# Optimization experiments

Hardware: AMD Instinct MI355X
Metric: run time of the kernel (lower is better)

Reference implementation:

```python
import jax, jax.numpy as jnp
import numpy as np
from jax.scipy.special import erf

N = 512          # n_points
S = 64           # steps
M = 32768        # number of events
MAX_TIME = 100.0
DELTA = MAX_TIME / S   # time_delta_size (torch.linspace gives uniform deltas)
EPS = 1e-12


def setup_inputs() -> dict:
    key = jax.random.key(0)
    k1, k2, k3, k4 = jax.random.split(key, 4)
    times = jnp.sort(jax.random.uniform(k1, (M,), dtype=jnp.float32) * MAX_TIME)
    ij = jax.random.randint(k2, (M, 2), 0, N).astype(jnp.float32)
    data = jnp.concatenate([ij, times[:, None]], axis=1)  # [node_i, node_j, time]
    z0 = jax.random.uniform(k3, (N, 2), dtype=jnp.float32) * 0.5
    v0 = jax.random.uniform(k4, (N, 2, S), dtype=jnp.float32) * 0.5
    beta = jnp.ones((1, 1), dtype=jnp.float32)
    return {
        "data": data,
        "t0": jnp.zeros((1,), dtype=jnp.float32),
        "tn": jnp.full((1,), MAX_TIME, dtype=jnp.float32),
        "z0": z0,
        "v0": v0,
        "beta": beta,
    }


def _forward(data, z0, v0, beta):
    times = data[:, 2]                      # (M,) assumed sorted, in [0, MAX_TIME]
    b = beta[0, 0]

    # --- time-step bucketing (vectorized version of the Python list-comp/np.unique) ---
    step_f = jnp.floor(times / DELTA)       # floored step value
    idx = jnp.clip(step_f, 0, S - 1).astype(jnp.int32)  # 't if t < steps else t-1'

    # piecewise-constant-velocity cumulative positions: (N, 2, S+1)
    Z_steps = jnp.concatenate(
        [z0[:, :, None], z0[:, :, None] + jnp.cumsum(v0 * DELTA, axis=2)], axis=2
    )

    # latent positions at each event time: (N, 2, M)
    dd = times - step_f * DELTA             # offset within the step
    Zt = Z_steps[:, :, idx] + v0[:, :, idx] * dd

    # --- event intensity: sum_{i<j} sum_e (beta - ||Zt_i - Zt_j||^2) ---
    # sum over events of d_ij computed via one small-K GEMM instead of (N,N,M)
    G = jnp.einsum('ndm,kdm->nk', Zt, Zt)   # (N, N)
    sq = jnp.diagonal(G)                    # sum_{d,m} Zt_i^2
    Dsum = sq[:, None] + sq[None, :] - 2.0 * G   # sum_e ||Zt_i - Zt_j||^2
    tri = jnp.triu(jnp.ones((N, N), dtype=bool), k=1)
    event_intensity = jnp.sum(jnp.where(tri, b * M - Dsum, 0.0))

    # --- unique occupied steps: first event per step, interval [ts, tf) ---
    pos = jnp.arange(M)
    first_pos = jax.ops.segment_min(pos, idx, num_segments=S)  # INT_MAX if empty
    occ = first_pos < M
    ts = times[jnp.clip(first_pos, 0, M - 1)]  # (S,), junk where not occupied

    # tf[s] = ts of next occupied step, last occupied step gets times[-1]
    def body(carry, x):
        ts_s, occ_s = x
        out = carry
        carry = jnp.where(occ_s, ts_s, carry)
        return carry, out
    _, tf_rev = jax.lax.scan(body, times[M - 1], (ts[::-1], occ[::-1]))
    tf = tf_rev[::-1]

    # --- analytic non-event integral over each occupied step ---
    # integral_{ts}^{tf} exp(beta - ||dz + dv*(t - ts)||^2) dt per node pair
    Z0s = Z_steps[:, :, :S]                 # step-start positions (N, 2, S)
    zz = jnp.einsum('nds,nds->ns', Z0s, Z0s)
    zv = jnp.einsum('nds,nds->ns', Z0s, v0)
    vv = jnp.einsum('nds,nds->ns', v0, v0)
    Czz = jnp.einsum('nds,mds->nms', Z0s, Z0s)
    Czv = jnp.einsum('nds,mds->nms', Z0s, v0)
    Cvv = jnp.einsum('nds,mds->nms', v0, v0)
    q = zz[:, None] + zz[None, :] - 2.0 * Czz               # ||dz||^2, (N,N,S)
    p = zv[:, None] + zv[None, :] - Czv - jnp.transpose(Czv, (1, 0, 2))  # dz.dv
    r = jnp.sqrt(vv[:, None] + vv[None, :] - 2.0 * Cvv + EPS)            # ||dv||

    T = tf - ts                              # (S,) interval lengths
    por = p / r
    integ = (jnp.exp(b - q + por * por) * (jnp.sqrt(jnp.pi) / (2.0 * r))
             * (erf(r * T + por) - erf(por)))             # (N,N,S)
    integ = jnp.where(occ[None, None, :], integ, 0.0)
    non_event_intensity = jnp.sum(jnp.where(tri, jnp.sum(integ, axis=2), 0.0))

    return event_intensity - non_event_intensity


def reference(data, t0, tn, z0, v0, beta):
    # t0 / tn are accepted by forward() but unused in its body
    return _forward(data, z0, v0, beta)
```

## Files before the change

### kernel.cpp

```cpp
#include <hip/hip_runtime.h>
#include <hip/hip_bf16.h>
#include <math.h>

#define N_NODES 512
#define S_STEPS 64
#define M_EV    32768
#define DELTA_F 1.5625f
#define TILE    16
#define NT      (N_NODES / TILE)
#define NOFF    (NT * (NT - 1) / 2)
#define NBLK    (NOFF + NT / 2)
#define SCHUNK  16
#define GLW1    0.21132486540518713f
#define GLW2    0.78867513459481287f


__device__ __forceinline__ int bucket_key(float t) {
    float stepf = floorf(t / DELTA_F);
    float cl = fminf(fmaxf(stepf, 0.f), 63.f);
    return (int)cl;
}

__device__ __forceinline__ int lower_bound_key(const float* __restrict__ data, int target) {
    int lo = 0, len = M_EV;
    while (len > 0) {
        int half = len >> 1;
        int mid = lo + half;
        if (bucket_key(data[3 * mid + 2]) < target) { lo = mid + 1; len -= half + 1; }
        else { len = half; }
    }
    return lo;
}

__global__ __launch_bounds__(256) void bucket_stats(const float* __restrict__ data,
                                                    float4* __restrict__ ws_c4) {
    int s   = blockIdx.x;
    int tid = threadIdx.x;
    __shared__ int sLo, sHi;
    __shared__ int   wcnt[4];
    __shared__ float wsdd[4], wsdd2[4];

    if (tid == 0)  sLo = lower_bound_key(data, s);
    if (tid == 64) sHi = lower_bound_key(data, s + 1);
    __syncthreads();
    int lo = sLo, hi = sHi;

    int   cnt = 0;
    float sdd = 0.f, sdd2 = 0.f;
    for (int m = lo + tid; m < hi; m += 256) {
        float t = data[3 * m + 2];
        float stepf = floorf(t / DELTA_F);
        float dd = t - stepf * DELTA_F;
        cnt++; sdd += dd; sdd2 += dd * dd;
    }
    for (int off = 32; off; off >>= 1) {
        cnt  += __shfl_down(cnt,  off);
        sdd  += __shfl_down(sdd,  off);
        sdd2 += __shfl_down(sdd2, off);
    }
    int wave = tid >> 6;
    if ((tid & 63) == 0) { wcnt[wave] = cnt; wsdd[wave] = sdd; wsdd2[wave] = sdd2; }
    __syncthreads();
    if (tid == 0) {
        int   c  = wcnt[0] + wcnt[1] + wcnt[2] + wcnt[3];
        float s1 = wsdd[0] + wsdd[1] + wsdd[2] + wsdd[3];
        float s2 = wsdd2[0] + wsdd2[1] + wsdd2[2] + wsdd2[3];
        float ts = data[3 * min(lo, M_EV - 1) + 2];
        float tf = data[3 * min(hi, M_EV - 1) + 2];
        float T  = (c > 0) ? (tf - ts) : 0.f;
        float t1 = T * GLW1, t2 = T * GLW2;
        ws_c4[s]      = make_float4((float)c, 2.f * s1, s2, 0.5f * T);
        ws_c4[64 + s] = make_float4(t1, t2, t1 * t1, t2 * t2);
    }
}

__global__ __launch_bounds__(1024, 8) void pair_kernel(
        const float* __restrict__ z0, const float* __restrict__ v0,
        const float* __restrict__ beta, const float4* __restrict__ ws_c4,
        double* __restrict__ partials) {
    __shared__ float4 Pi[S_STEPS][17];
    __shared__ float4 Pj[S_STEPS][17];
    __shared__ float4 sC[128];
    __shared__ double wD[16], wI[16];

    int l = blockIdx.x;
    bool isDiag = (l >= NOFF);
    int it, jt;
    if (!isDiag) {
        int it_ = 0, rem = l;
        while (rem >= NT - 1 - it_) { rem -= NT - 1 - it_; ++it_; }
        it = it_; jt = it_ + 1 + rem;
    } else {
        int k = l - NOFF;
        it = 2 * k; jt = 2 * k + 1;
    }

    int tid  = threadIdx.x;
    int wave = tid >> 6, lane = tid & 63;

    if (tid < 128) sC[tid] = ws_c4[tid];

    for (int e = wave * 2; e < wave * 2 + 2; ++e) {
        int loc = e & 15;
        int n = (e < 16 ? it : jt) * TILE + loc;
        float vx = v0[n * 128 + lane];
        float vy = v0[n * 128 + 64 + lane];
        float ix = vx, iy = vy;
        #pragma unroll
        for (int off = 1; off < 64; off <<= 1) {
            float ux = __shfl_up(ix, off);
            float uy = __shfl_up(iy, off);
            if (lane >= off) { ix += ux; iy += uy; }
        }
        float zx = fmaf(DELTA_F, ix - vx, z0[2 * n]);
        float zy = fmaf(DELTA_F, iy - vy, z0[2 * n + 1]);
        float4 val = make_float4(zx, zy, vx, vy);
        if (e < 16) Pi[lane][loc] = val; else Pj[lane][loc] = val;
    }
    __syncthreads();

    int chunk = tid >> 8;
    int r  = tid & 255;
    int li = r >> 4, lj = r & 15;

    const float4* rowA;
    const float4* rowB;
    bool act;
    if (!isDiag) {
        rowA = &Pi[0][li]; rowB = &Pj[0][lj]; act = true;
    } else if (li < lj) {
        rowA = &Pi[0][li]; rowB = &Pi[0][lj]; act = true;
    } else {
        int bb = min(li + 1, 15);
        rowA = &Pj[0][lj]; rowB = &Pj[0][bb]; act = (li < 15);
    }

    float accD = 0.f, accI = 0.f;
    float b = beta[0];

    if (act) {
        int s0 = chunk * SCHUNK;
        const float4* pA = rowA + s0 * 17;
        const float4* pB = rowB + s0 * 17;
        const float4* pK1 = &sC[s0];
        const float4* pK2 = &sC[64 + s0];
        #pragma unroll 4
        for (int ss = 0; ss < SCHUNK; ++ss) {
            float4 a  = pA[ss * 17];
            float4 c  = pB[ss * 17];
            float4 k1 = pK1[ss];
            float4 k2 = pK2[ss];
            float dx  = a.x - c.x,  dy  = a.y - c.y;
            float dvx = a.z - c.z,  dvy = a.w - c.w;
            float q  = dx * dx + dy * dy;
            float p  = fmaf(dx, dvx, dy * dvy);
            float vv = fmaf(dvx, dvx, dvy * dvy);
            accD += fmaf(k1.x, q, fmaf(k1.y, p, k1.z * vv));
            float bq = b - q;
            float p2 = p + p;
            float e1 = fmaf(-k2.x, p2, fmaf(-k2.z, vv, bq));
            float e2 = fmaf(-k2.y, p2, fmaf(-k2.w, vv, bq));
            accI = fmaf(k1.w, __expf(e1) + __expf(e2), accI);
        }
    }

    for (int off = 32; off; off >>= 1) {
        accD += __shfl_down(accD, off);
        accI += __shfl_down(accI, off);
    }
    if (lane == 0) { wD[wave] = (double)accD; wI[wave] = (double)accI; }
    __syncthreads();
    if (tid == 0) {
        double D = 0.0, I = 0.0;
        #pragma unroll
        for (int k = 0; k < 16; ++k) { D += wD[k]; I += wI[k]; }
        partials[2 * l]     = D;
        partials[2 * l + 1] = I;
    }
}

__global__ void final_reduce(const float* __restrict__ beta,
                             const double* __restrict__ partials,
                             float* __restrict__ out) {
    __shared__ double sD[256], sI[256];
    int tid = threadIdx.x;
    double dD = 0.0, dI = 0.0;
    for (int l = tid; l < NBLK; l += 256) {
        dD += partials[2 * l];
        dI += partials[2 * l + 1];
    }
    sD[tid] = dD; sI[tid] = dI;
    __syncthreads();
    for (int off = 128; off; off >>= 1) {
        if (tid < off) { sD[tid] += sD[tid + off]; sI[tid] += sI[tid + off]; }
        __syncthreads();
    }
    if (tid == 0) {
        double npairs = (double)N_NODES * (double)(N_NODES - 1) * 0.5;
        double ev = (double)beta[0] * (double)M_EV * npairs - sD[0];
        out[0] = (float)(ev - sI[0]);
    }
}

extern "C" void kernel_launch(void* const* d_in, const int* in_sizes, int n_in,
                              void* d_out, int out_size, void* d_ws, size_t ws_size,
                              hipStream_t stream) {
    const float* data = (const float*)d_in[0];
    const float* z0   = (const float*)d_in[3];
    const float* v0   = (const float*)d_in[4];
    const float* beta = (const float*)d_in[5];

    float4* ws_c4    = (float4*)d_ws;
    double* partials = (double*)((char*)d_ws + 4096);
    float*  out      = (float*)d_out;

    bucket_stats<<<64, 256, 0, stream>>>(data, ws_c4);
    pair_kernel<<<NBLK, 1024, 0, stream>>>(z0, v0, beta, ws_c4, partials);
    final_reduce<<<1, 256, 0, stream>>>(beta, partials, out);
}
```

Before: 24.99 us.

## Compute two pairs per thread with wave-uniform scalar constant loads

Each thread now handles two i-rows against one shared j-column over 8 steps, where before it handled one pair over 16 steps. This lets the j-side LDS read be reused across both pairs. The per-step constants are read straight from global memory using a readfirstlane'd wave-uniform index, so they can become scalar loads, and the shared-memory staging of constants is removed. The diagonal tiles keep per-pair predication, which adds code size and divergence in exchange for fewer LDS reads on the common off-diagonal path.

```diff
diff --git a/kernel.cpp b/kernel.cpp
--- a/kernel.cpp
+++ b/kernel.cpp
@@ -10,7 +10,6 @@
 #define NT      (N_NODES / TILE)
 #define NOFF    (NT * (NT - 1) / 2)
 #define NBLK    (NOFF + NT / 2)
-#define SCHUNK  16
 #define GLW1    0.21132486540518713f
 #define GLW2    0.78867513459481287f
 
@@ -74,13 +73,37 @@
     }
 }
 
+__device__ __forceinline__ void dual_step(const float4 a0, const float4 a1, const float4 c,
+                                          const float4 k1, const float4 k2, float b,
+                                          float& accD, float& accI) {
+    float dx0  = a0.x - c.x,  dy0  = a0.y - c.y;
+    float dvx0 = a0.z - c.z,  dvy0 = a0.w - c.w;
+    float dx1  = a1.x - c.x,  dy1  = a1.y - c.y;
+    float dvx1 = a1.z - c.z,  dvy1 = a1.w - c.w;
+    float q0  = dx0 * dx0 + dy0 * dy0;
+    float q1  = dx1 * dx1 + dy1 * dy1;
+    float p0  = fmaf(dx0, dvx0, dy0 * dvy0);
+    float p1  = fmaf(dx1, dvx1, dy1 * dvy1);
+    float vv0 = fmaf(dvx0, dvx0, dvy0 * dvy0);
+    float vv1 = fmaf(dvx1, dvx1, dvy1 * dvy1);
+    accD += fmaf(k1.x, q0, fmaf(k1.y, p0, k1.z * vv0));
+    accD += fmaf(k1.x, q1, fmaf(k1.y, p1, k1.z * vv1));
+    float bq0 = b - q0, bq1 = b - q1;
+    float p20 = p0 + p0, p21 = p1 + p1;
+    float e10 = fmaf(-k2.x, p20, fmaf(-k2.z, vv0, bq0));
+    float e20 = fmaf(-k2.y, p20, fmaf(-k2.w, vv0, bq0));
+    float e11 = fmaf(-k2.x, p21, fmaf(-k2.z, vv1, bq1));
+    float e21 = fmaf(-k2.y, p21, fmaf(-k2.w, vv1, bq1));
+    accI = fmaf(k1.w, __expf(e10) + __expf(e20), accI);
+    accI = fmaf(k1.w, __expf(e11) + __expf(e21), accI);
+}
+
 __global__ __launch_bounds__(1024, 8) void pair_kernel(
         const float* __restrict__ z0, const float* __restrict__ v0,
         const float* __restrict__ beta, const float4* __restrict__ ws_c4,
         double* __restrict__ partials) {
     __shared__ float4 Pi[S_STEPS][17];
     __shared__ float4 Pj[S_STEPS][17];
-    __shared__ float4 sC[128];
     __shared__ double wD[16], wI[16];
 
     int l = blockIdx.x;
@@ -98,8 +121,6 @@
     int tid  = threadIdx.x;
     int wave = tid >> 6, lane = tid & 63;
 
-    if (tid < 128) sC[tid] = ws_c4[tid];
-
     for (int e = wave * 2; e < wave * 2 + 2; ++e) {
         int loc = e & 15;
         int n = (e < 16 ? it : jt) * TILE + loc;
@@ -119,48 +140,61 @@
     }
     __syncthreads();
 
-    int chunk = tid >> 8;
-    int r  = tid & 255;
-    int li = r >> 4, lj = r & 15;
-
-    const float4* rowA;
-    const float4* rowB;
-    bool act;
+    int chunk = tid >> 7;
+    int r   = tid & 127;
+    int lj  = r & 15;
+    int li0 = r >> 4;
+    int li1 = li0 + 8;
+
+    float accD = 0.f, accI = 0.f;
+    float b  = beta[0];
+    int sbase = __builtin_amdgcn_readfirstlane(chunk * 8);
+
     if (!isDiag) {
-        rowA = &Pi[0][li]; rowB = &Pj[0][lj]; act = true;
-    } else if (li < lj) {
-        rowA = &Pi[0][li]; rowB = &Pi[0][lj]; act = true;
+        const float4* pA0 = &Pi[sbase][li0];
+        const float4* pA1 = &Pi[sbase][li1];
+        const float4* pC  = &Pj[sbase][lj];
+        #pragma unroll
+        for (int ss = 0; ss < 8; ++ss) {
+            float4 k1 = ws_c4[sbase + ss];
+            float4 k2 = ws_c4[64 + sbase + ss];
+            dual_step(pA0[ss * 17], pA1[ss * 17], pC[ss * 17], k1, k2, b, accD, accI);
+        }
     } else {
-        int bb = min(li + 1, 15);
-        rowA = &Pj[0][lj]; rowB = &Pj[0][bb]; act = (li < 15);
-    }
-
-    float accD = 0.f, accI = 0.f;
-    float b = beta[0];
-
-    if (act) {
-        int s0 = chunk * SCHUNK;
-        const float4* pA = rowA + s0 * 17;
-        const float4* pB = rowB + s0 * 17;
-        const float4* pK1 = &sC[s0];
-        const float4* pK2 = &sC[64 + s0];
-        #pragma unroll 4
-        for (int ss = 0; ss < SCHUNK; ++ss) {
-            float4 a  = pA[ss * 17];
-            float4 c  = pB[ss * 17];
-            float4 k1 = pK1[ss];
-            float4 k2 = pK2[ss];
-            float dx  = a.x - c.x,  dy  = a.y - c.y;
-            float dvx = a.z - c.z,  dvy = a.w - c.w;
-            float q  = dx * dx + dy * dy;
-            float p  = fmaf(dx, dvx, dy * dvy);
-            float vv = fmaf(dvx, dvx, dvy * dvy);
-            accD += fmaf(k1.x, q, fmaf(k1.y, p, k1.z * vv));
-            float bq = b - q;
-            float p2 = p + p;
-            float e1 = fmaf(-k2.x, p2, fmaf(-k2.z, vv, bq));
-            float e2 = fmaf(-k2.y, p2, fmaf(-k2.w, vv, bq));
-            accI = fmaf(k1.w, __expf(e1) + __expf(e2), accI);
+        const float4 *rA0, *rB0, *rA1, *rB1;
+        bool act0, act1;
+        if (li0 < lj) { rA0 = &Pi[sbase][li0]; rB0 = &Pi[sbase][lj]; act0 = true; }
+        else { int bb = min(li0 + 1, 15); rA0 = &Pj[sbase][lj]; rB0 = &Pj[sbase][bb]; act0 = (li0 < 15); }
+        if (li1 < lj) { rA1 = &Pi[sbase][li1]; rB1 = &Pi[sbase][lj]; act1 = true; }
+        else { int bb = min(li1 + 1, 15); rA1 = &Pj[sbase][lj]; rB1 = &Pj[sbase][bb]; act1 = (li1 < 15); }
+        #pragma unroll
+        for (int ss = 0; ss < 8; ++ss) {
+            float4 k1 = ws_c4[sbase + ss];
+            float4 k2 = ws_c4[64 + sbase + ss];
+            if (act0) {
+                float4 a = rA0[ss * 17], c = rB0[ss * 17];
+                float dx = a.x - c.x, dy = a.y - c.y, dvx = a.z - c.z, dvy = a.w - c.w;
+                float q = dx * dx + dy * dy;
+                float p = fmaf(dx, dvx, dy * dvy);
+                float vv = fmaf(dvx, dvx, dvy * dvy);
+                accD += fmaf(k1.x, q, fmaf(k1.y, p, k1.z * vv));
+                float bq = b - q, p2 = p + p;
+                float e1 = fmaf(-k2.x, p2, fmaf(-k2.z, vv, bq));
+                float e2 = fmaf(-k2.y, p2, fmaf(-k2.w, vv, bq));
+                accI = fmaf(k1.w, __expf(e1) + __expf(e2), accI);
+            }
+            if (act1) {
+                float4 a = rA1[ss * 17], c = rB1[ss * 17];
+                float dx = a.x - c.x, dy = a.y - c.y, dvx = a.z - c.z, dvy = a.w - c.w;
+                float q = dx * dx + dy * dy;
+                float p = fmaf(dx, dvx, dy * dvy);
+                float vv = fmaf(dvx, dvx, dvy * dvy);
+                accD += fmaf(k1.x, q, fmaf(k1.y, p, k1.z * vv));
+                float bq = b - q, p2 = p + p;
+                float e1 = fmaf(-k2.x, p2, fmaf(-k2.z, vv, bq));
+                float e2 = fmaf(-k2.y, p2, fmaf(-k2.w, vv, bq));
+                accI = fmaf(k1.w, __expf(e1) + __expf(e2), accI);
+            }
         }
     }
 
```

Measured after the change: 21.53 us. -13.8%, faster.

## Precompute step positions once, register-tile pair loop, parallelize bucket search

Applied to the files above, without the earlier changes.

Cumulative step positions are now computed once per node in a prep kernel and written to a workspace slab, so pair blocks no longer redo the prefix scan for every tile. The pair loop gives each thread a 2x2 register tile of node pairs over 4 steps, reusing each loaded row twice, and reads step constants directly from global memory instead of staging them in shared memory. The serial binary search for bucket bounds becomes a coarse parallel sample plus a fine 128-wide scan, folded into the same prep kernel. The risks are extra global traffic for the slab and more divergence on the diagonal blocks.

```diff
diff --git a/kernel.cpp b/kernel.cpp
--- a/kernel.cpp
+++ b/kernel.cpp
@@ -10,9 +10,9 @@
 #define NT      (N_NODES / TILE)
 #define NOFF    (NT * (NT - 1) / 2)
 #define NBLK    (NOFF + NT / 2)
-#define SCHUNK  16
 #define GLW1    0.21132486540518713f
 #define GLW2    0.78867513459481287f
+#define INF_I   0x7fffffff
 
 
 __device__ __forceinline__ int bucket_key(float t) {
@@ -21,45 +21,83 @@
     return (int)cl;
 }
 
-__device__ __forceinline__ int lower_bound_key(const float* __restrict__ data, int target) {
-    int lo = 0, len = M_EV;
-    while (len > 0) {
-        int half = len >> 1;
-        int mid = lo + half;
-        if (bucket_key(data[3 * mid + 2]) < target) { lo = mid + 1; len -= half + 1; }
-        else { len = half; }
-    }
-    return lo;
-}
-
-__global__ __launch_bounds__(256) void bucket_stats(const float* __restrict__ data,
-                                                    float4* __restrict__ ws_c4) {
-    int s   = blockIdx.x;
-    int tid = threadIdx.x;
+__global__ __launch_bounds__(1024) void prep(const float* __restrict__ data,
+                                             const float* __restrict__ z0,
+                                             const float* __restrict__ v0,
+                                             float4* __restrict__ ws_c4,
+                                             float2* __restrict__ slabZ) {
+    int blk = blockIdx.x, tid = threadIdx.x;
+    int wave = tid >> 6, lane = tid & 63;
+
+    {
+        int nd = blk * 16 + wave;
+        int n = nd >> 1, d = nd & 1;
+        float v = v0[n * 128 + d * 64 + lane];
+        float ix = v;
+        #pragma unroll
+        for (int off = 1; off < 64; off <<= 1) {
+            float u = __shfl_up(ix, off);
+            if (lane >= off) ix += u;
+        }
+        float z = fmaf(DELTA_F, ix - v, z0[2 * n + d]);
+        ((float*)slabZ)[(n * 64 + lane) * 2 + d] = z;
+    }
+
+    __shared__ int redA[4], redB[4];
     __shared__ int sLo, sHi;
     __shared__ int   wcnt[4];
     __shared__ float wsdd[4], wsdd2[4];
-
-    if (tid == 0)  sLo = lower_bound_key(data, s);
-    if (tid == 64) sHi = lower_bound_key(data, s + 1);
+    int s = blk;
+
+    if (tid < 256) {
+        int m = tid << 7;
+        int key = bucket_key(data[3 * m + 2]);
+        int cl = (key >= s)     ? m : INF_I;
+        int ch = (key >= s + 1) ? m : INF_I;
+        for (int off = 32; off; off >>= 1) {
+            cl = min(cl, __shfl_down(cl, off));
+            ch = min(ch, __shfl_down(ch, off));
+        }
+        if (lane == 0) { redA[wave] = cl; redB[wave] = ch; }
+    }
+    __syncthreads();
+    if (tid < 256) {
+        int posL = min(min(redA[0], redA[1]), min(redA[2], redA[3]));
+        int posH = min(min(redB[0], redB[1]), min(redB[2], redB[3]));
+        if (posL == INF_I) posL = M_EV;
+        if (posH == INF_I) posH = M_EV;
+        int base = (tid < 128) ? posL : posH;
+        int tgt  = (tid < 128) ? s : s + 1;
+        int m2 = base - 127 + (tid & 127);
+        int cand = INF_I;
+        if (m2 >= 0 && m2 < M_EV && bucket_key(data[3 * m2 + 2]) >= tgt) cand = m2;
+        for (int off = 32; off; off >>= 1) cand = min(cand, __shfl_down(cand, off));
+        if (lane == 0) redA[wave] = cand;
+    }
+    __syncthreads();
+    if (tid == 0) {
+        int lo = min(redA[0], redA[1]); if (lo == INF_I) lo = M_EV;
+        int hi = min(redA[2], redA[3]); if (hi == INF_I) hi = M_EV;
+        sLo = lo; sHi = hi;
+    }
     __syncthreads();
     int lo = sLo, hi = sHi;
-
-    int   cnt = 0;
-    float sdd = 0.f, sdd2 = 0.f;
-    for (int m = lo + tid; m < hi; m += 256) {
-        float t = data[3 * m + 2];
-        float stepf = floorf(t / DELTA_F);
-        float dd = t - stepf * DELTA_F;
-        cnt++; sdd += dd; sdd2 += dd * dd;
-    }
-    for (int off = 32; off; off >>= 1) {
-        cnt  += __shfl_down(cnt,  off);
-        sdd  += __shfl_down(sdd,  off);
-        sdd2 += __shfl_down(sdd2, off);
-    }
-    int wave = tid >> 6;
-    if ((tid & 63) == 0) { wcnt[wave] = cnt; wsdd[wave] = sdd; wsdd2[wave] = sdd2; }
+    if (tid < 256) {
+        int   cnt = 0;
+        float sdd = 0.f, sdd2 = 0.f;
+        for (int m = lo + tid; m < hi; m += 256) {
+            float t = data[3 * m + 2];
+            float stepf = floorf(t / DELTA_F);
+            float dd = t - stepf * DELTA_F;
+            cnt++; sdd += dd; sdd2 += dd * dd;
+        }
+        for (int off = 32; off; off >>= 1) {
+            cnt  += __shfl_down(cnt,  off);
+            sdd  += __shfl_down(sdd,  off);
+            sdd2 += __shfl_down(sdd2, off);
+        }
+        if (lane == 0) { wcnt[wave] = cnt; wsdd[wave] = sdd; wsdd2[wave] = sdd2; }
+    }
     __syncthreads();
     if (tid == 0) {
         int   c  = wcnt[0] + wcnt[1] + wcnt[2] + wcnt[3];
@@ -74,13 +112,27 @@
     }
 }
 
+__device__ __forceinline__ void one_step(const float4 a, const float4 c,
+                                         const float4 k1, const float4 k2, float b,
+                                         float& accD, float& accI) {
+    float dx  = a.x - c.x,  dy  = a.y - c.y;
+    float dvx = a.z - c.z,  dvy = a.w - c.w;
+    float q  = dx * dx + dy * dy;
+    float p  = fmaf(dx, dvx, dy * dvy);
+    float vv = fmaf(dvx, dvx, dvy * dvy);
+    accD += fmaf(k1.x, q, fmaf(k1.y, p, k1.z * vv));
+    float bq = b - q, p2 = p + p;
+    float e1 = fmaf(-k2.x, p2, fmaf(-k2.z, vv, bq));
+    float e2 = fmaf(-k2.y, p2, fmaf(-k2.w, vv, bq));
+    accI = fmaf(k1.w, __expf(e1) + __expf(e2), accI);
+}
+
 __global__ __launch_bounds__(1024, 8) void pair_kernel(
-        const float* __restrict__ z0, const float* __restrict__ v0,
-        const float* __restrict__ beta, const float4* __restrict__ ws_c4,
+        const float* __restrict__ v0, const float* __restrict__ beta,
+        const float4* __restrict__ ws_c4, const float2* __restrict__ slabZ,
         double* __restrict__ partials) {
     __shared__ float4 Pi[S_STEPS][17];
     __shared__ float4 Pj[S_STEPS][17];
-    __shared__ float4 sC[128];
     __shared__ double wD[16], wI[16];
 
     int l = blockIdx.x;
@@ -98,69 +150,63 @@
     int tid  = threadIdx.x;
     int wave = tid >> 6, lane = tid & 63;
 
-    if (tid < 128) sC[tid] = ws_c4[tid];
-
-    for (int e = wave * 2; e < wave * 2 + 2; ++e) {
-        int loc = e & 15;
-        int n = (e < 16 ? it : jt) * TILE + loc;
-        float vx = v0[n * 128 + lane];
-        float vy = v0[n * 128 + 64 + lane];
-        float ix = vx, iy = vy;
-        #pragma unroll
-        for (int off = 1; off < 64; off <<= 1) {
-            float ux = __shfl_up(ix, off);
-            float uy = __shfl_up(iy, off);
-            if (lane >= off) { ix += ux; iy += uy; }
-        }
-        float zx = fmaf(DELTA_F, ix - vx, z0[2 * n]);
-        float zy = fmaf(DELTA_F, iy - vy, z0[2 * n + 1]);
-        float4 val = make_float4(zx, zy, vx, vy);
-        if (e < 16) Pi[lane][loc] = val; else Pj[lane][loc] = val;
-    }
-    __syncthreads();
-
-    int chunk = tid >> 8;
-    int r  = tid & 255;
-    int li = r >> 4, lj = r & 15;
-
-    const float4* rowA;
-    const float4* rowB;
-    bool act;
-    if (!isDiag) {
-        rowA = &Pi[0][li]; rowB = &Pj[0][lj]; act = true;
-    } else if (li < lj) {
-        rowA = &Pi[0][li]; rowB = &Pi[0][lj]; act = true;
-    } else {
-        int bb = min(li + 1, 15);
-        rowA = &Pj[0][lj]; rowB = &Pj[0][bb]; act = (li < 15);
-    }
+    #pragma unroll
+    for (int p = 0; p < 2; ++p) {
+        int e   = tid + p * 1024;
+        int s   = e & 63;
+        int loc = (e >> 6) & 15;
+        int n = (p == 0 ? it : jt) * TILE + loc;
+        float2 zz = slabZ[n * 64 + s];
+        float  vx = v0[n * 128 + s];
+        float  vy = v0[n * 128 + 64 + s];
+        float4 val = make_float4(zz.x, zz.y, vx, vy);
+        if (p == 0) Pi[s][loc] = val; else Pj[s][loc] = val;
+    }
+    __syncthreads();
+
+    int sbase = __builtin_amdgcn_readfirstlane((tid >> 6) * 4);
+    int r   = tid & 63;
+    int li0 = r >> 3, li1 = li0 + 8;
+    int lj0 = r & 7,  lj1 = lj0 + 8;
 
     float accD = 0.f, accI = 0.f;
     float b = beta[0];
 
-    if (act) {
-        int s0 = chunk * SCHUNK;
-        const float4* pA = rowA + s0 * 17;
-        const float4* pB = rowB + s0 * 17;
-        const float4* pK1 = &sC[s0];
-        const float4* pK2 = &sC[64 + s0];
-        #pragma unroll 4
-        for (int ss = 0; ss < SCHUNK; ++ss) {
-            float4 a  = pA[ss * 17];
-            float4 c  = pB[ss * 17];
-            float4 k1 = pK1[ss];
-            float4 k2 = pK2[ss];
-            float dx  = a.x - c.x,  dy  = a.y - c.y;
-            float dvx = a.z - c.z,  dvy = a.w - c.w;
-            float q  = dx * dx + dy * dy;
-            float p  = fmaf(dx, dvx, dy * dvy);
-            float vv = fmaf(dvx, dvx, dvy * dvy);
-            accD += fmaf(k1.x, q, fmaf(k1.y, p, k1.z * vv));
-            float bq = b - q;
-            float p2 = p + p;
-            float e1 = fmaf(-k2.x, p2, fmaf(-k2.z, vv, bq));
-            float e2 = fmaf(-k2.y, p2, fmaf(-k2.w, vv, bq));
-            accI = fmaf(k1.w, __expf(e1) + __expf(e2), accI);
+    if (!isDiag) {
+        const float4* pA0 = &Pi[sbase][li0];
+        const float4* pA1 = &Pi[sbase][li1];
+        const float4* pC0 = &Pj[sbase][lj0];
+        const float4* pC1 = &Pj[sbase][lj1];
+        #pragma unroll
+        for (int ss = 0; ss < 4; ++ss) {
+            float4 k1 = ws_c4[sbase + ss];
+            float4 k2 = ws_c4[64 + sbase + ss];
+            float4 a0 = pA0[ss * 17], a1 = pA1[ss * 17];
+            float4 c0 = pC0[ss * 17], c1 = pC1[ss * 17];
+            one_step(a0, c0, k1, k2, b, accD, accI);
+            one_step(a0, c1, k1, k2, b, accD, accI);
+            one_step(a1, c0, k1, k2, b, accD, accI);
+            one_step(a1, c1, k1, k2, b, accD, accI);
+        }
+    } else {
+        const float4 *A0, *B0, *A1, *B1, *A2, *B2, *A3, *B3;
+        bool g0, g1, g2, g3;
+        #define DECODE(X, Y, A, B, G) \
+            if ((X) < (Y)) { A = &Pi[sbase][X]; B = &Pi[sbase][Y]; G = true; } \
+            else { int bb_ = min((X) + 1, 15); A = &Pj[sbase][Y]; B = &Pj[sbase][bb_]; G = ((X) < 15); }
+        DECODE(li0, lj0, A0, B0, g0)
+        DECODE(li0, lj1, A1, B1, g1)
+        DECODE(li1, lj0, A2, B2, g2)
+        DECODE(li1, lj1, A3, B3, g3)
+        #undef DECODE
+        #pragma unroll
+        for (int ss = 0; ss < 4; ++ss) {
+            float4 k1 = ws_c4[sbase + ss];
+            float4 k2 = ws_c4[64 + sbase + ss];
+            if (g0) one_step(A0[ss * 17], B0[ss * 17], k1, k2, b, accD, accI);
+            if (g1) one_step(A1[ss * 17], B1[ss * 17], k1, k2, b, accD, accI);
+            if (g2) one_step(A2[ss * 17], B2[ss * 17], k1, k2, b, accD, accI);
+            if (g3) one_step(A3[ss * 17], B3[ss * 17], k1, k2, b, accD, accI);
         }
     }
 
@@ -211,10 +257,11 @@
     const float* beta = (const float*)d_in[5];
 
     float4* ws_c4    = (float4*)d_ws;
-    double* partials = (double*)((char*)d_ws + 4096);
+    double* partials = (double*)((char*)d_ws + 2048);
+    float2* slabZ    = (float2*)((char*)d_ws + 16384);
     float*  out      = (float*)d_out;
 
-    bucket_stats<<<64, 256, 0, stream>>>(data, ws_c4);
-    pair_kernel<<<NBLK, 1024, 0, stream>>>(z0, v0, beta, ws_c4, partials);
+    prep<<<64, 1024, 0, stream>>>(data, z0, v0, ws_c4, slabZ);
+    pair_kernel<<<NBLK, 1024, 0, stream>>>(v0, beta, ws_c4, slabZ, partials);
     final_reduce<<<1, 256, 0, stream>>>(beta, partials, out);
 }
```

New measurement: 20.72 us, median of 2. -17.1%, faster.
